# Optimization experiments

Hardware: AMD Instinct MI355X
Metric: run time of the kernel (lower is better)

## Reference

```python
import jax, jax.numpy as jnp
import numpy as np

DIM = 64
POS_H = 64
ATTN_H = 4 * DIM
B, N = 2, 512


def setup_inputs() -> dict:
    key = jax.random.key(0)
    ks = jax.random.split(key, 20)
    g = lambda k, shape, fan_in: jax.random.normal(k, shape, jnp.float32) / np.sqrt(fan_in)
    return {
        "x": jax.random.normal(ks[0], (B, N, DIM), jnp.float32),
        "pos": jax.random.normal(ks[1], (B, N, 3), jnp.float32),
        "prev_w": g(ks[2], (DIM, DIM), DIM), "prev_b": jnp.zeros((DIM,), jnp.float32),
        "q_w": g(ks[3], (DIM, DIM), DIM),
        "k_w": g(ks[4], (DIM, DIM), DIM),
        "v_w": g(ks[5], (DIM, DIM), DIM),
        "pos_w1": g(ks[6], (3, POS_H), 3), "pos_b1": jnp.zeros((POS_H,), jnp.float32),
        "pos_w2": g(ks[7], (POS_H, DIM), POS_H), "pos_b2": jnp.zeros((DIM,), jnp.float32),
        "attn_w1": g(ks[8], (DIM, ATTN_H), DIM), "attn_b1": jnp.zeros((ATTN_H,), jnp.float32),
        "attn_w2": g(ks[9], (ATTN_H, DIM), ATTN_H), "attn_b2": jnp.zeros((DIM,), jnp.float32),
        "fin_w": g(ks[10], (DIM, DIM), DIM), "fin_b": jnp.zeros((DIM,), jnp.float32),
    }


def reference(x, pos, prev_w, prev_b, q_w, k_w, v_w,
              pos_w1, pos_b1, pos_w2, pos_b2,
              attn_w1, attn_b1, attn_w2, attn_b2, fin_w, fin_b):
    # prev_linear
    x1 = x @ prev_w + prev_b                              # [B,N,D]
    q = x1 @ q_w                                          # [B,N,D]
    k = x1 @ k_w
    v = x1 @ v_w
    # relative position embedding: [B,i,j,3] -> MLP -> [B,i,j,D]
    rel_pos = pos[:, :, None, :] - pos[:, None, :, :]
    rpe = jax.nn.relu(rel_pos @ pos_w1 + pos_b1) @ pos_w2 + pos_b2
    # per-pair qk difference + attn MLP -> vector (channel-wise) attention logits
    qk_rel = q[:, :, None, :] - k[:, None, :, :]          # [B,i,j,D]
    sim = jax.nn.relu((qk_rel + rpe) @ attn_w1 + attn_b1) @ attn_w2 + attn_b2  # [B,i,j,D]
    # v indexed by j, plus pairwise positional embedding
    v2 = v[:, None, :, :] + rpe                           # [B,i,j,D]
    attn = jax.nn.softmax(sim, axis=2)                    # softmax over j (dim=-2 of [B,i,j,D])
    agg = jnp.einsum('bijd,bijd->bid', attn, v2)          # [B,N,D]
    x_out = agg @ fin_w + fin_b + x1                      # final_linear + residual
    return (x_out, pos)
```

## Files before the change

kernel.cpp:

```cpp
#include <hip/hip_runtime.h>

typedef __attribute__((ext_vector_type(4))) float f32x4;
typedef __attribute__((ext_vector_type(8))) __bf16 bf16x8;
typedef __attribute__((ext_vector_type(4))) __bf16 bf16x4;
typedef __attribute__((ext_vector_type(2))) unsigned int u32x2;

template<int OFF>
__device__ __forceinline__ u32x2 tr_read_o(unsigned base){
    u32x2 d;
    asm volatile("ds_read_b64_tr_b16 %0, %1 offset:%c2"
                 : "=v"(d) : "v"(base), "i"(OFF));
    return d;
}
__device__ __forceinline__ bf16x8 frag_cat(u32x2 a, u32x2 b){
    union { u32x2 u[2]; bf16x8 f; } c; c.u[0] = a; c.u[1] = b; return c.f;
}


__global__ void ptb_pre(const float* __restrict__ x,
                        const float* __restrict__ pos,
                        const float* __restrict__ prev_w,
                        const float* __restrict__ prev_b,
                        const float* __restrict__ q_w,
                        const float* __restrict__ k_w,
                        const float* __restrict__ v_w,
                        const float* __restrict__ pos_w2,
                        const float* __restrict__ attn_w1,
                        const float* __restrict__ attn_b1,
                        float* __restrict__ ws,
                        float* __restrict__ out)
{
    const int bid = blockIdx.x;
    const int tid = threadIdx.x;
    __shared__ float xr[256], x1r[256], qsh[256], ksh[256], vsh[256];

    float wcol[64];
    #pragma unroll
    for (int c = 0; c < 64; ++c) wcol[c] = attn_w1[c*256 + tid];

    if (bid >= 256){
        xr[tid] = pos_w2[(bid - 256)*256 + tid];
        __syncthreads();
        float* Wp = ws + 655360;
        #pragma unroll
        for (int r = 0; r < 4; ++r){
            float s = 0.f;
            #pragma unroll 16
            for (int c = 0; c < 64; ++c) s += xr[r*64 + c] * wcol[c];
            Wp[((bid - 256)*4 + r)*256 + tid] = s;
        }
        return;
    }

    const int rr  = tid >> 6, d = tid & 63;
    const int row = bid*4 + rr;
    xr[tid] = x[row*64 + d];
    __syncthreads();
    float a = prev_b[d];
    #pragma unroll 16
    for (int c = 0; c < 64; ++c) a += xr[rr*64 + c] * prev_w[c*64 + d];
    x1r[tid] = a;
    ws[row*64 + d] = a;
    __syncthreads();
    float qv = 0.f, kv = 0.f, vv = 0.f;
    #pragma unroll 16
    for (int c = 0; c < 64; ++c){
        float t = x1r[rr*64 + c];
        qv += t * q_w[c*64 + d];
        kv += t * k_w[c*64 + d];
        vv += t * v_w[c*64 + d];
    }
    qsh[tid] = qv; ksh[tid] = kv; vsh[tid] = vv;
    if (tid < 12) out[65536 + bid*12 + tid] = pos[bid*12 + tid];
    __syncthreads();

    ws[65536 + bid*256 + tid] = vsh[(tid & 3)*64 + (tid >> 2)];

    float* Q1  = ws + 131072;
    float* K1s = ws + 393216;
    const float bb = attn_b1[tid];
    float sq[4], sk[4];
    #pragma unroll
    for (int r = 0; r < 4; ++r){ sq[r] = bb; sk[r] = 0.f; }
    #pragma unroll 16
    for (int c = 0; c < 64; ++c){
        const float wv = wcol[c];
        #pragma unroll
        for (int r = 0; r < 4; ++r){
            sq[r] += qsh[r*64 + c] * wv;
            sk[r] += ksh[r*64 + c] * wv;
        }
    }
    #pragma unroll
    for (int r = 0; r < 4; ++r) Q1[(bid*4 + r)*256 + tid] = sq[r];
    f32x4 kvec = {sk[0], sk[1], sk[2], sk[3]};
    *(f32x4*)&K1s[bid*1024 + tid*4] = kvec;
}

__global__ __launch_bounds__(256) void ptb_main(
    const float* __restrict__ pos,
    const float* __restrict__ pos_w1, const float* __restrict__ pos_b1,
    const float* __restrict__ pos_w2, const float* __restrict__ pos_b2,
    const float* __restrict__ attn_w2, const float* __restrict__ attn_b2,
    const float* __restrict__ fin_w, const float* __restrict__ fin_b,
    const float* __restrict__ ws, float* __restrict__ out)
{
    const int blk = blockIdx.x;
    const int b   = blk >> 9;
    const int i   = blk & 511;
    const int tid = threadIdx.x;
    const int w   = tid >> 6;
    const int l   = tid & 63;
    const int lg  = l >> 4;
    const int ln  = l & 15;

    __shared__ __bf16 sH1[2][64][64];
    __shared__ __bf16 sHT[64][2][4][16];
    __shared__ float sPW1[192], sPB1[64], sAGG[64], sPOSI[3];

    const float* x1p = ws;
    const float* vs  = ws + 65536;
    const float* Q1  = ws + 131072;
    const float* K1s = ws + 393216;
    const float* Wp  = ws + 655360;

    if (tid < 64) sPB1[tid] = pos_b1[tid];
    if (tid >= 64 && tid < 256) sPW1[tid - 64] = pos_w1[tid - 64];
    if (tid < 3) sPOSI[tid] = pos[(b*512 + i)*3 + tid];

    const int dch  = w*16 + ln;
    const int Ew   = w*64;
    const int swzA = (ln & 7) << 3;

    bf16x8 w1f[2][4];
    #pragma unroll
    for (int kf = 0; kf < 2; ++kf)
        #pragma unroll
        for (int et = 0; et < 4; ++et)
            #pragma unroll
            for (int ii = 0; ii < 8; ++ii)
                w1f[kf][et][ii] = (__bf16)Wp[(kf*32 + lg*8 + ii)*256 + Ew + et*16 + ln];
    bf16x8 w2f[8];
    #pragma unroll
    for (int kf = 0; kf < 8; ++kf)
        #pragma unroll
        for (int ii = 0; ii < 8; ++ii)
            w2f[kf][ii] = (__bf16)attn_w2[(kf*32 + lg*8 + ii)*64 + dch];
    bf16x8 pwfw[2];
    #pragma unroll
    for (int kf = 0; kf < 2; ++kf)
        #pragma unroll
        for (int ii = 0; ii < 8; ++ii)
            pwfw[kf][ii] = (__bf16)pos_w2[(kf*32 + lg*8 + ii)*64 + dch];

    float Q1b[4];
    #pragma unroll
    for (int et = 0; et < 4; ++et) Q1b[et] = Q1[blk*256 + Ew + et*16 + ln];
    const float pb2v = pos_b2[dch];
    const float b2v  = attn_b2[dch];

    const unsigned sHTb = (unsigned)(unsigned long long)&sHT[0][0][0][0];
    const unsigned trbase = sHTb + (unsigned)(lg*512 + ln*8);

    float mrun = -1e30f, srun = 0.f, arun = 0.f;

    auto stageA = [&](int j0a){
        const int bufa = (j0a >> 6) & 1;
        const float* pj = &pos[(b*512 + j0a + w*16 + ln)*3];
        const float r0 = sPOSI[0] - pj[0];
        const float r1 = sPOSI[1] - pj[1];
        const float r2 = sPOSI[2] - pj[2];
        #pragma unroll
        for (int kf = 0; kf < 2; ++kf){
            const int hb = kf*32 + lg*8;
            f32x4 wa0 = *(const f32x4*)&sPW1[      hb],   wa1 = *(const f32x4*)&sPW1[      hb+4];
            f32x4 wb0 = *(const f32x4*)&sPW1[ 64 + hb],   wb1 = *(const f32x4*)&sPW1[ 64 + hb+4];
            f32x4 wc0 = *(const f32x4*)&sPW1[128 + hb],   wc1 = *(const f32x4*)&sPW1[128 + hb+4];
            f32x4 bb0 = *(const f32x4*)&sPB1[      hb],   bb1 = *(const f32x4*)&sPB1[      hb+4];
            bf16x8 h1f;
            #pragma unroll
            for (int ii = 0; ii < 4; ++ii){
                float hv0 = bb0[ii] + r0*wa0[ii] + r1*wb0[ii] + r2*wc0[ii];
                float hv1 = bb1[ii] + r0*wa1[ii] + r1*wb1[ii] + r2*wc1[ii];
                h1f[ii]   = (__bf16)fmaxf(hv0, 0.f);
                h1f[ii+4] = (__bf16)fmaxf(hv1, 0.f);
            }
            *(bf16x8*)&sH1[bufa][w*16 + ln][hb ^ swzA] = h1f;
        }
    };

    __syncthreads();
    stageA(0);

    #pragma unroll 1
    for (int t = 0; t < 8; ++t){
        const int j0  = t << 6;
        const int buf = t & 1;
        __syncthreads();
        if (t < 7) stageA(j0 + 64);
        #pragma unroll 1
        for (int hb = 0; hb < 2; ++hb){
            f32x4 rcs[2];
            #pragma unroll
            for (int jj = 0; jj < 2; ++jj){
                const int jrow = hb*32 + jj*16;
                const int krow = ((b*512 + j0 + jrow) >> 2) + lg;
                const bf16x8 af0 = *(const bf16x8*)&sH1[buf][jrow + ln][(     lg*8) ^ swzA];
                const bf16x8 af1 = *(const bf16x8*)&sH1[buf][jrow + ln][(32 + lg*8) ^ swzA];
                f32x4 accs[4];
                #pragma unroll
                for (int et = 0; et < 4; ++et){
                    const f32x4 kw4 = *(const f32x4*)&K1s[krow*1024 + (Ew + et*16 + ln)*4];
                    const f32x4 qv4 = {Q1b[et], Q1b[et], Q1b[et], Q1b[et]};
                    accs[et] = qv4 - kw4;
                }
                __builtin_amdgcn_s_setprio(1);
                #pragma unroll
                for (int et = 0; et < 4; ++et)
                    accs[et] = __builtin_amdgcn_mfma_f32_16x16x32_bf16(af0, w1f[0][et], accs[et], 0, 0, 0);
                #pragma unroll
                for (int et = 0; et < 4; ++et)
                    accs[et] = __builtin_amdgcn_mfma_f32_16x16x32_bf16(af1, w1f[1][et], accs[et], 0, 0, 0);
                f32x4 rcv = {pb2v, pb2v, pb2v, pb2v};
                rcv = __builtin_amdgcn_mfma_f32_16x16x32_bf16(af0, pwfw[0], rcv, 0, 0, 0);
                rcv = __builtin_amdgcn_mfma_f32_16x16x32_bf16(af1, pwfw[1], rcv, 0, 0, 0);
                rcs[jj] = rcv;
                __builtin_amdgcn_s_setprio(0);
                #pragma unroll
                for (int et = 0; et < 4; ++et){
                    bf16x4 hp;
                    #pragma unroll
                    for (int ri = 0; ri < 4; ++ri) hp[ri] = (__bf16)fmaxf(accs[et][ri], 0.f);
                    *(bf16x4*)&sHT[w*16 + et*4 + (ln>>2)][jj][ln&3][lg*4] = hp;
                }
            }
            __syncthreads();
            #pragma unroll
            for (int jj = 0; jj < 2; ++jj){
                const int jrow = hb*32 + jj*16;
                const int vrow = ((b*512 + j0 + jrow) >> 2) + lg;
                const f32x4 vv4 = *(const f32x4*)&vs[vrow*256 + dch*4];
                const unsigned trb = trbase + (unsigned)(jj*128);
                u32x2 hh[16];
                if (jj == 0){
                    #define TR2(KF) \
                        hh[(KF)*2]   = tr_read_o<(KF)*2048      >(trb); \
                        hh[(KF)*2+1] = tr_read_o<(KF)*2048 + 256>(trb);
                    TR2(0) TR2(1) TR2(2) TR2(3) TR2(4) TR2(5) TR2(6) TR2(7)
                    #undef TR2
                } else {
                    #define TR2(KF) \
                        hh[(KF)*2]   = tr_read_o<(KF)*2048 + 128>(trb - 128u); \
                        hh[(KF)*2+1] = tr_read_o<(KF)*2048 + 384>(trb - 128u);
                    TR2(0) TR2(1) TR2(2) TR2(3) TR2(4) TR2(5) TR2(6) TR2(7)
                    #undef TR2
                }
                asm volatile("s_waitcnt lgkmcnt(8)" ::: "memory");
                __builtin_amdgcn_sched_barrier(0);
                f32x4 a0 = {b2v, b2v, b2v, b2v};
                f32x4 a1 = {0.f, 0.f, 0.f, 0.f};
                __builtin_amdgcn_s_setprio(1);
                a0 = __builtin_amdgcn_mfma_f32_16x16x32_bf16(frag_cat(hh[0], hh[1]), w2f[0], a0, 0, 0, 0);
                a1 = __builtin_amdgcn_mfma_f32_16x16x32_bf16(frag_cat(hh[2], hh[3]), w2f[1], a1, 0, 0, 0);
                a0 = __builtin_amdgcn_mfma_f32_16x16x32_bf16(frag_cat(hh[4], hh[5]), w2f[2], a0, 0, 0, 0);
                a1 = __builtin_amdgcn_mfma_f32_16x16x32_bf16(frag_cat(hh[6], hh[7]), w2f[3], a1, 0, 0, 0);
                __builtin_amdgcn_s_setprio(0);
                asm volatile("s_waitcnt lgkmcnt(0)" ::: "memory");
                __builtin_amdgcn_sched_barrier(0);
                __builtin_amdgcn_s_setprio(1);
                a0 = __builtin_amdgcn_mfma_f32_16x16x32_bf16(frag_cat(hh[8],  hh[9]),  w2f[4], a0, 0, 0, 0);
                a1 = __builtin_amdgcn_mfma_f32_16x16x32_bf16(frag_cat(hh[10], hh[11]), w2f[5], a1, 0, 0, 0);
                a0 = __builtin_amdgcn_mfma_f32_16x16x32_bf16(frag_cat(hh[12], hh[13]), w2f[6], a0, 0, 0, 0);
                a1 = __builtin_amdgcn_mfma_f32_16x16x32_bf16(frag_cat(hh[14], hh[15]), w2f[7], a1, 0, 0, 0);
                __builtin_amdgcn_s_setprio(0);
                const f32x4 acc = a0 + a1;
                const f32x4 rc  = rcs[jj];
                float tmax = fmaxf(fmaxf(acc[0], acc[1]), fmaxf(acc[2], acc[3]));
                tmax = fmaxf(tmax, __shfl_xor(tmax, 16));
                tmax = fmaxf(tmax, __shfl_xor(tmax, 32));
                const float mnew  = fmaxf(mrun, tmax);
                const float scale = __expf(mrun - mnew);
                srun *= scale; arun *= scale; mrun = mnew;
                #pragma unroll
                for (int ri = 0; ri < 4; ++ri){
                    const float p = __expf(acc[ri] - mnew);
                    srun += p;
                    arun += p * (vv4[ri] + rc[ri]);
                }
            }
            if (hb == 0) __syncthreads();
        }
    }

    arun += __shfl_xor(arun, 16); arun += __shfl_xor(arun, 32);
    srun += __shfl_xor(srun, 16); srun += __shfl_xor(srun, 32);
    if (lg == 0) sAGG[dch] = arun / srun;
    __syncthreads();

    if (tid < 64){
        float a = fin_b[tid] + x1p[blk*64 + tid];
        #pragma unroll 16
        for (int c = 0; c < 64; ++c) a += sAGG[c] * fin_w[c*64 + tid];
        out[blk*64 + tid] = a;
    }
}

extern "C" void kernel_launch(void* const* d_in, const int* in_sizes, int n_in,
                              void* d_out, int out_size, void* d_ws, size_t ws_size,
                              hipStream_t stream)
{
    const float* x       = (const float*)d_in[0];
    const float* pos     = (const float*)d_in[1];
    const float* prev_w  = (const float*)d_in[2];
    const float* prev_b  = (const float*)d_in[3];
    const float* q_w     = (const float*)d_in[4];
    const float* k_w     = (const float*)d_in[5];
    const float* v_w     = (const float*)d_in[6];
    const float* pos_w1  = (const float*)d_in[7];
    const float* pos_b1  = (const float*)d_in[8];
    const float* pos_w2  = (const float*)d_in[9];
    const float* pos_b2  = (const float*)d_in[10];
    const float* attn_w1 = (const float*)d_in[11];
    const float* attn_b1 = (const float*)d_in[12];
    const float* attn_w2 = (const float*)d_in[13];
    const float* attn_b2 = (const float*)d_in[14];
    const float* fin_w   = (const float*)d_in[15];
    const float* fin_b   = (const float*)d_in[16];
    float* out = (float*)d_out;
    float* ws  = (float*)d_ws;

    ptb_pre<<<272, 256, 0, stream>>>(x, pos, prev_w, prev_b, q_w, k_w, v_w,
                                     pos_w2, attn_w1, attn_b1, ws, out);
    ptb_main<<<1024, 256, 0, stream>>>(pos, pos_w1, pos_b1, pos_w2, pos_b2,
                                       attn_w2, attn_b2, fin_w, fin_b, ws, out);
}
```

Before: 110.7 us.

## Pad transposed hidden LDS buffer, hoist V loads, merge online-softmax updates

Changes the sHT shared buffer from a dense [64][2][4][16] bf16 array to a padded byte layout with a 144-byte row stride and separate jj halves. This is meant to cut LDS bank conflicts on the bf16x4 stores and the ds_read_b64_tr_b16 transposed reads. It also issues both V global loads before the MFMA loop, and does one online-softmax max/rescale per pair of 16-row tiles instead of one per tile. The padding adds shared memory, which may affect occupancy, and the merged softmax keeps more accumulators live.

```diff
diff --git a/kernel.cpp b/kernel.cpp
--- a/kernel.cpp
+++ b/kernel.cpp
@@ -115,7 +115,7 @@
     const int ln  = l & 15;
 
     __shared__ __bf16 sH1[2][64][64];
-    __shared__ __bf16 sHT[64][2][4][16];
+    __shared__ __align__(16) char sHT[18432];
     __shared__ float sPW1[192], sPB1[64], sAGG[64], sPOSI[3];
 
     const float* x1p = ws;
@@ -159,8 +159,8 @@
     const float pb2v = pos_b2[dch];
     const float b2v  = attn_b2[dch];
 
-    const unsigned sHTb = (unsigned)(unsigned long long)&sHT[0][0][0][0];
-    const unsigned trbase = sHTb + (unsigned)(lg*512 + ln*8);
+    const unsigned sHTb = (unsigned)(unsigned long long)&sHT[0];
+    const unsigned trbase = sHTb + (unsigned)(lg*288 + ln*8);
 
     float mrun = -1e30f, srun = 0.f, arun = 0.f;
 
@@ -231,30 +231,26 @@
                     bf16x4 hp;
                     #pragma unroll
                     for (int ri = 0; ri < 4; ++ri) hp[ri] = (__bf16)fmaxf(accs[et][ri], 0.f);
-                    *(bf16x4*)&sHT[w*16 + et*4 + (ln>>2)][jj][ln&3][lg*4] = hp;
+                    *(bf16x4*)(sHT + (jj*64 + w*16 + et*4 + (ln>>2))*144
+                                   + (ln&3)*32 + lg*8) = hp;
                 }
             }
             __syncthreads();
+            f32x4 accv[2], vvv[2];
             #pragma unroll
             for (int jj = 0; jj < 2; ++jj){
-                const int jrow = hb*32 + jj*16;
-                const int vrow = ((b*512 + j0 + jrow) >> 2) + lg;
-                const f32x4 vv4 = *(const f32x4*)&vs[vrow*256 + dch*4];
-                const unsigned trb = trbase + (unsigned)(jj*128);
+                const int vrow = ((b*512 + j0 + hb*32 + jj*16) >> 2) + lg;
+                vvv[jj] = *(const f32x4*)&vs[vrow*256 + dch*4];
+            }
+            #pragma unroll
+            for (int jj = 0; jj < 2; ++jj){
+                const unsigned trb = trbase + (unsigned)(jj*9216);
                 u32x2 hh[16];
-                if (jj == 0){
-                    #define TR2(KF) \
-                        hh[(KF)*2]   = tr_read_o<(KF)*2048      >(trb); \
-                        hh[(KF)*2+1] = tr_read_o<(KF)*2048 + 256>(trb);
-                    TR2(0) TR2(1) TR2(2) TR2(3) TR2(4) TR2(5) TR2(6) TR2(7)
-                    #undef TR2
-                } else {
-                    #define TR2(KF) \
-                        hh[(KF)*2]   = tr_read_o<(KF)*2048 + 128>(trb - 128u); \
-                        hh[(KF)*2+1] = tr_read_o<(KF)*2048 + 384>(trb - 128u);
-                    TR2(0) TR2(1) TR2(2) TR2(3) TR2(4) TR2(5) TR2(6) TR2(7)
-                    #undef TR2
-                }
+                #define TR2(KF) \
+                    hh[(KF)*2]   = tr_read_o<(KF)*1152      >(trb); \
+                    hh[(KF)*2+1] = tr_read_o<(KF)*1152 + 144>(trb);
+                TR2(0) TR2(1) TR2(2) TR2(3) TR2(4) TR2(5) TR2(6) TR2(7)
+                #undef TR2
                 asm volatile("s_waitcnt lgkmcnt(8)" ::: "memory");
                 __builtin_amdgcn_sched_barrier(0);
                 f32x4 a0 = {b2v, b2v, b2v, b2v};
@@ -273,21 +269,25 @@
                 a0 = __builtin_amdgcn_mfma_f32_16x16x32_bf16(frag_cat(hh[12], hh[13]), w2f[6], a0, 0, 0, 0);
                 a1 = __builtin_amdgcn_mfma_f32_16x16x32_bf16(frag_cat(hh[14], hh[15]), w2f[7], a1, 0, 0, 0);
                 __builtin_amdgcn_s_setprio(0);
-                const f32x4 acc = a0 + a1;
-                const f32x4 rc  = rcs[jj];
-                float tmax = fmaxf(fmaxf(acc[0], acc[1]), fmaxf(acc[2], acc[3]));
-                tmax = fmaxf(tmax, __shfl_xor(tmax, 16));
-                tmax = fmaxf(tmax, __shfl_xor(tmax, 32));
-                const float mnew  = fmaxf(mrun, tmax);
-                const float scale = __expf(mrun - mnew);
-                srun *= scale; arun *= scale; mrun = mnew;
+                accv[jj] = a0 + a1;
+            }
+            float tmax = fmaxf(fmaxf(fmaxf(accv[0][0], accv[0][1]),
+                                     fmaxf(accv[0][2], accv[0][3])),
+                               fmaxf(fmaxf(accv[1][0], accv[1][1]),
+                                     fmaxf(accv[1][2], accv[1][3])));
+            tmax = fmaxf(tmax, __shfl_xor(tmax, 16));
+            tmax = fmaxf(tmax, __shfl_xor(tmax, 32));
+            const float mnew  = fmaxf(mrun, tmax);
+            const float scale = __expf(mrun - mnew);
+            srun *= scale; arun *= scale; mrun = mnew;
+            #pragma unroll
+            for (int jj = 0; jj < 2; ++jj)
                 #pragma unroll
                 for (int ri = 0; ri < 4; ++ri){
-                    const float p = __expf(acc[ri] - mnew);
+                    const float p = __expf(accv[jj][ri] - mnew);
                     srun += p;
-                    arun += p * (vv4[ri] + rc[ri]);
+                    arun += p * (vvv[jj][ri] + rcs[jj][ri]);
                 }
-            }
             if (hb == 0) __syncthreads();
         }
     }
```

New measurement: 106.7 us. 3.6% less time.
